# Performance work log

Measured on AMD Instinct MI355X. Metric: run time of the kernel, lower is better.

## Reference

```python
import jax, jax.numpy as jnp
import numpy as np

NUM_HEADS = 4
LN_EPS = 1e-5
L2_EPS = 1e-12


def setup_inputs() -> dict:
    key = jax.random.key(0)
    ks = jax.random.split(key, 10)
    B, L, D, Hd = 256, 197, 768, 512
    dh = Hd // NUM_HEADS  # 128
    NC = 1000
    sc = lambda k, shape, s: jax.random.normal(k, shape, jnp.float32) * s
    return {
        "cls_token": jax.random.normal(ks[0], (B, D), jnp.float32),
        "x": jax.random.normal(ks[1], (B, L, D), jnp.float32),
        "proj_w": sc(ks[2], (D, Hd), 0.02),
        "proj_b": jnp.zeros((Hd,), jnp.float32),
        "ln_g": jnp.ones((dh,), jnp.float32),
        "ln_b": jnp.zeros((dh,), jnp.float32),
        "conv1_w": sc(ks[3], (3, 3, 3, 3), 0.2),
        "conv2_w": sc(ks[4], (3, 3, 3, 3), 0.2),
        "cls1_w": sc(ks[5], (D, NC), 0.02),
        "cls1_b": jnp.zeros((NC,), jnp.float32),
        "cls2_w": sc(ks[6], (2883, NC), 0.02),
        "cls2_b": jnp.zeros((NC,), jnp.float32),
    }


def reference(cls_token, x, proj_w, proj_b, ln_g, ln_b, conv1_w, conv2_w,
              cls1_w, cls1_b, cls2_w, cls2_b):
    B, L, D = x.shape
    dh = ln_g.shape[0]
    # proj on patch tokens (drop cls at position 0)
    xp = x[:, 1:, :] @ proj_w + proj_b            # (B, 196, 512)
    Lp = xp.shape[1]
    H = xp.shape[2] // dh
    heads = xp.reshape(B, Lp, H, dh).transpose(2, 0, 1, 3)  # (H, B, Lp, dh)
    # LayerNorm over last dim (eps=1e-5, biased var, affine)
    mu = heads.mean(-1, keepdims=True)
    var = heads.var(-1, keepdims=True)
    hn = (heads - mu) * jax.lax.rsqrt(var + LN_EPS) * ln_g + ln_b
    # Covariance._remove_mean: adaptive_avg_pool2d on (B, dh, Lp) -> mean over BOTH dh and Lp per sample
    hn = hn - hn.mean(axis=(2, 3), keepdims=True)
    # 'near' cross-covariances between adjacent heads, all pairs batched
    x1, x2 = hn[:-1], hn[1:]                      # (H-1, B, Lp, dh)
    cov = jnp.einsum('pbnd,pbne->pbde', x1, x2) / Lp  # (H-1, B, dh, dh)
    # L2 normalize over dim=2 (row axis of each dh x dh map), F.normalize eps
    nrm = jnp.sqrt(jnp.sum(cov * cov, axis=2, keepdims=True))
    cov = cov / jnp.maximum(nrm, L2_EPS)
    cov = cov.transpose(1, 0, 2, 3)               # (B, 3, 128, 128)
    conv = lambda z, w: jax.lax.conv_general_dilated(
        z, w, (2, 2), 'VALID', dimension_numbers=('NCHW', 'OIHW', 'NCHW'))
    z = conv(cov, conv1_w)                        # (B, 3, 63, 63)
    z = jax.nn.gelu(z, approximate=False)
    z = conv(z, conv2_w)                          # (B, 3, 31, 31)
    flat = z.reshape(B, -1)                       # (B, 2883)
    out = ((cls_token @ cls1_w + cls1_b) + (flat @ cls2_w + cls2_b)) / 2
    return out
```

## Files before the change

kernel.cpp:

```cpp
#include <hip/hip_runtime.h>
#include <hip/hip_bf16.h>
#include <cstdint>

typedef __bf16 bf16_t;
typedef __bf16 bf16x4 __attribute__((ext_vector_type(4)));
typedef __bf16 bf16x8 __attribute__((ext_vector_type(8)));
typedef float floatx4 __attribute__((ext_vector_type(4)));

#define LNEPS 1e-5f

__device__ inline void async_copy16(const bf16_t* g, bf16_t* l) {
    __builtin_amdgcn_global_load_lds((const __attribute__((address_space(1))) void*)g,
                                     (__attribute__((address_space(3))) void*)l,
                                     16, 0, 0);
}

__global__ __launch_bounds__(256)
void k_cvt_x(const float* __restrict__ x, bf16_t* __restrict__ xbf) {
    const int vid = blockIdx.x * 256 + threadIdx.x;
    const int row = vid / 96;
    const int kv  = vid - row * 96;
    const int b = row / 196, l = row - (row / 196) * 196;
    const float* src = x + ((b * 197 + l + 1) * 96 + kv) * 8;
    const floatx4 f0 = *(const floatx4*)src;
    const floatx4 f1 = *(const floatx4*)(src + 4);
    bf16x8 o;
#pragma unroll
    for (int e = 0; e < 4; e++) { o[e] = (bf16_t)f0[e]; o[e+4] = (bf16_t)f1[e]; }
    *(bf16x8*)(xbf + vid * 8) = o;
}

__global__ __launch_bounds__(256)
void k_transpose_w(const float* __restrict__ w, bf16_t* __restrict__ wt) {
    __shared__ bf16_t tile[32][33];
    const int bx = blockIdx.x;
    const int by = blockIdx.y;
    const int tx = threadIdx.x & 31, ty = threadIdx.x >> 5;
    for (int i = ty; i < 32; i += 8)
        tile[i][tx] = (bf16_t)w[(by*32 + i)*512 + bx*32 + tx];
    __syncthreads();
    for (int i = ty; i < 32; i += 8)
        wt[(bx*32 + i)*768 + by*32 + tx] = tile[tx][i];
}

__global__ __launch_bounds__(256, 3)
void k_proj_ln(const bf16_t* __restrict__ xbf, const bf16_t* __restrict__ wt,
               const float* __restrict__ pb, const float* __restrict__ lng,
               const float* __restrict__ lnb, bf16_t* __restrict__ hn,
               float* __restrict__ csum)
{
    __shared__ bf16_t As[3][128*32];
    __shared__ bf16_t Bs[3][128*32];

    const int t = threadIdx.x;
    const int lane = t & 63;
    const int wv = t >> 6;
    const int q = lane >> 4;
    const int c = lane & 15;
    const int L = blockIdx.x;
    const int xcd = L & 7, slot = L >> 3;
    const int h = slot & 3;
    const int m0 = (xcd + 8 * (slot >> 2)) * 128;

    const int srow  = t >> 2;
    const int skoff = (t & 3) * 8;
    const bf16_t* ag = xbf + (m0 + srow) * 768 + skoff;
    const bf16_t* bg = wt + (h*128 + srow) * 768 + skoff;

#define STAGE(B, kk)                                                     \
    {                                                                    \
        const int kn_ = (kk) * 32;                                       \
        async_copy16(ag + kn_,          &As[B][t*8]);                    \
        async_copy16(ag + 64*768 + kn_, &As[B][2048 + t*8]);             \
        async_copy16(bg + kn_,          &Bs[B][t*8]);                    \
        async_copy16(bg + 64*768 + kn_, &Bs[B][2048 + t*8]);             \
    }

#define COMPUTE(B)                                                       \
    {                                                                    \
        bf16x8 af[2], bfr[8];                                            \
        _Pragma("unroll")                                                \
        for (int i = 0; i < 2; i++)                                      \
            af[i] = *(const bf16x8*)&As[B][(wv*32 + i*16 + c)*32 + q*8]; \
        _Pragma("unroll")                                                \
        for (int j = 0; j < 8; j++)                                      \
            bfr[j] = *(const bf16x8*)&Bs[B][(j*16 + c)*32 + q*8];        \
        _Pragma("unroll")                                                \
        for (int i = 0; i < 2; i++)                                      \
            _Pragma("unroll")                                            \
            for (int j = 0; j < 8; j++)                                  \
                acc[i][j] = __builtin_amdgcn_mfma_f32_16x16x32_bf16(af[i], bfr[j], acc[i][j], 0, 0, 0); \
    }

    floatx4 acc[2][8];
#pragma unroll
    for (int i = 0; i < 2; i++)
#pragma unroll
        for (int j = 0; j < 8; j++)
#pragma unroll
            for (int r = 0; r < 4; r++) acc[i][j][r] = 0.f;

    STAGE(0, 0);
    STAGE(1, 1);
    STAGE(2, 2);

    for (int ks = 0; ks < 22; ks++) {
        const int buf = ks % 3;
        asm volatile("s_waitcnt vmcnt(8)" ::: "memory");
        __builtin_amdgcn_s_barrier();
        COMPUTE(buf);
        __builtin_amdgcn_s_barrier();
        if (ks < 21) STAGE(buf, ks + 3);
    }
    asm volatile("s_waitcnt vmcnt(4)" ::: "memory");
    __builtin_amdgcn_s_barrier();
    COMPUTE(1);
    __builtin_amdgcn_s_barrier();
    asm volatile("s_waitcnt vmcnt(0)" ::: "memory");
    __builtin_amdgcn_s_barrier();
    COMPUTE(2);

#undef STAGE
#undef COMPUTE

    float bias[8], gg[8], bb[8];
#pragma unroll
    for (int j = 0; j < 8; j++) {
        const int d = j*16 + c;
        bias[j] = pb[h*128 + d];
        gg[j]   = lng[d];
        bb[j]   = lnb[d];
    }
    float cs0[8], cs1[8];
#pragma unroll
    for (int j = 0; j < 8; j++) { cs0[j] = 0.f; cs1[j] = 0.f; }
    const int b0 = m0 / 196;
    const int bL = (m0 + 127) / 196;
#pragma unroll
    for (int i = 0; i < 2; i++) {
#pragma unroll
        for (int r = 0; r < 4; r++) {
            float s = 0.f, s2 = 0.f;
#pragma unroll
            for (int j = 0; j < 8; j++) {
                const float v = acc[i][j][r] + bias[j];
                acc[i][j][r] = v;
                s += v; s2 += v*v;
            }
#pragma unroll
            for (int o = 1; o < 16; o <<= 1) { s += __shfl_xor(s, o); s2 += __shfl_xor(s2, o); }
            const float mu = s * (1.f/128.f);
            const float ms = s2 * (1.f/128.f);
            const float rstd = rsqrtf(ms - mu*mu + LNEPS);
            const int gm = m0 + wv*32 + i*16 + q*4 + r;
            const int bI = gm / 196, l = gm - bI*196;
            bf16_t* dst = hn + (((h*256 + bI)*196 + l) << 7);
            const bool first = (bI == b0);
#pragma unroll
            for (int j = 0; j < 8; j++) {
                const float v = (acc[i][j][r] - mu)*rstd*gg[j] + bb[j];
                dst[j*16 + c] = (bf16_t)v;
                cs0[j] += first ? v : 0.f;
                cs1[j] += first ? 0.f : v;
            }
        }
    }
    float* scr = (float*)As;
#pragma unroll
    for (int j = 0; j < 8; j++) {
        float s0 = cs0[j], s1 = cs1[j];
        s0 += __shfl_xor(s0, 16); s0 += __shfl_xor(s0, 32);
        s1 += __shfl_xor(s1, 16); s1 += __shfl_xor(s1, 32);
        if (q == 0) {
            scr[(wv*2 + 0)*128 + j*16 + c] = s0;
            scr[(wv*2 + 1)*128 + j*16 + c] = s1;
        }
    }
    __syncthreads();
    {
        const int bucket = t >> 7, d = t & 127;
        if (bucket == 0 || bL > b0) {
            const float s = scr[(0*2 + bucket)*128 + d] + scr[(1*2 + bucket)*128 + d]
                          + scr[(2*2 + bucket)*128 + d] + scr[(3*2 + bucket)*128 + d];
            atomicAdd(&csum[((h*256 + b0 + bucket) << 7) + d], s);
        }
    }
}

__global__ __launch_bounds__(256, 2)
void k_cov(const bf16_t* __restrict__ hn, const float* __restrict__ colsum,
           float* __restrict__ cov)
{
    __shared__ bf16_t x1s[128*40];
    __shared__ bf16_t x2s[128*40];
    __shared__ float rs1[128], rs2[128];
    __shared__ float colsq[2][128];
    __shared__ float nrm_inv[128];
    __shared__ float mu_s[2];

    const int t = threadIdx.x;
    const int lane = t & 63;
    const int wv = t >> 6;
    const int wr = wv >> 1, wc = wv & 1;
    const int q = lane >> 4;
    const int c = lane & 15;
    const int b = blockIdx.x;
    const int p = blockIdx.y;

    const bf16_t* X1 = hn + (((p*256 + b)*196) << 7);
    const bf16_t* X2 = hn + ((((p+1)*256 + b)*196) << 7);

    if (t < 128) rs1[t] = colsum[((p*256 + b) << 7) + t];
    else         rs2[t & 127] = colsum[(((p+1)*256 + b) << 7) + (t & 127)];
    __syncthreads();
    if (wv == 0) {
        float s = rs1[lane] + rs1[lane + 64];
#pragma unroll
        for (int o = 1; o < 64; o <<= 1) s += __shfl_xor(s, o);
        if (lane == 0) mu_s[0] = s * (1.f/(196.f*128.f));
    } else if (wv == 1) {
        float s = rs2[lane] + rs2[lane + 64];
#pragma unroll
        for (int o = 1; o < 64; o <<= 1) s += __shfl_xor(s, o);
        if (lane == 0) mu_s[1] = s * (1.f/(196.f*128.f));
    }

    floatx4 acc[4][4];
#pragma unroll
    for (int i = 0; i < 4; i++)
#pragma unroll
        for (int j = 0; j < 4; j++)
#pragma unroll
            for (int r = 0; r < 4; r++) acc[i][j][r] = 0.f;

    const int nl = t >> 3;
    const int d0 = (t & 7) * 16;

    for (int n0 = 0; n0 < 224; n0 += 32) {
        __syncthreads();
        const int n = n0 + nl;
        bf16x8 va, vb, wa, wb;
        if (n < 196) {
            const bf16_t* s1 = X1 + (n << 7) + d0;
            const bf16_t* s2 = X2 + (n << 7) + d0;
            va = *(const bf16x8*)s1;
            vb = *(const bf16x8*)(s1 + 8);
            wa = *(const bf16x8*)s2;
            wb = *(const bf16x8*)(s2 + 8);
        } else {
#pragma unroll
            for (int e = 0; e < 8; e++) {
                va[e] = (bf16_t)0.f; vb[e] = (bf16_t)0.f;
                wa[e] = (bf16_t)0.f; wb[e] = (bf16_t)0.f;
            }
        }
#pragma unroll
        for (int e = 0; e < 8; e++) {
            x1s[(d0 + e)*40 + nl]     = va[e];
            x1s[(d0 + 8 + e)*40 + nl] = vb[e];
            x2s[(d0 + e)*40 + nl]     = wa[e];
            x2s[(d0 + 8 + e)*40 + nl] = wb[e];
        }
        __syncthreads();
        bf16x8 af[4], bfr[4];
#pragma unroll
        for (int i = 0; i < 4; i++)
            af[i] = *(const bf16x8*)&x1s[(wr*64 + i*16 + c)*40 + q*8];
#pragma unroll
        for (int j = 0; j < 4; j++)
            bfr[j] = *(const bf16x8*)&x2s[(wc*64 + j*16 + c)*40 + q*8];
#pragma unroll
        for (int i = 0; i < 4; i++)
#pragma unroll
            for (int j = 0; j < 4; j++)
                acc[i][j] = __builtin_amdgcn_mfma_f32_16x16x32_bf16(af[i], bfr[j], acc[i][j], 0, 0, 0);
    }

    const float mu1 = mu_s[0], mu2 = mu_s[1];
    const float invL = 1.f/196.f;
    float csq[4] = {0.f, 0.f, 0.f, 0.f};
#pragma unroll
    for (int i = 0; i < 4; i++)
#pragma unroll
        for (int j = 0; j < 4; j++)
#pragma unroll
            for (int r = 0; r < 4; r++) {
                const int d = wr*64 + i*16 + q*4 + r;
                const int e = wc*64 + j*16 + c;
                const float v = acc[i][j][r]*invL - mu2*rs1[d]*invL - mu1*rs2[e]*invL + mu1*mu2;
                acc[i][j][r] = v;
                csq[j] += v*v;
            }
#pragma unroll
    for (int j = 0; j < 4; j++) {
        float s = csq[j];
        s += __shfl_xor(s, 16);
        s += __shfl_xor(s, 32);
        csq[j] = s;
    }
    if (q == 0) {
#pragma unroll
        for (int j = 0; j < 4; j++) colsq[wr][wc*64 + j*16 + c] = csq[j];
    }
    __syncthreads();
    if (t < 128) {
        const float nr = sqrtf(colsq[0][t] + colsq[1][t]);
        nrm_inv[t] = 1.f / fmaxf(nr, 1e-12f);
    }
    __syncthreads();
    float* dst = cov + ((long)b*3 + p)*16384;
#pragma unroll
    for (int i = 0; i < 4; i++)
#pragma unroll
        for (int j = 0; j < 4; j++) {
            const int e = wc*64 + j*16 + c;
            const float ni = nrm_inv[e];
#pragma unroll
            for (int r = 0; r < 4; r++) {
                const int d = wr*64 + i*16 + q*4 + r;
                dst[(d << 7) + e] = acc[i][j][r] * ni;
            }
        }
}

__global__ __launch_bounds__(256)
void k_convs(const float* __restrict__ cov, const float* __restrict__ w1,
             const float* __restrict__ w2, bf16_t* __restrict__ Xb)
{
    __shared__ float Z[3*33*63];
    __shared__ float W1s[81];
    __shared__ float W2s[81];
    const int t = threadIdx.x;
    const int b = blockIdx.x >> 1, half = blockIdx.x & 1;
    const int zy0 = half ? 32 : 0;
    const int nzy = half ? 31 : 33;
    const int y20 = half ? 16 : 0;
    const int ny2 = half ? 15 : 16;
    if (t < 81) { W1s[t] = w1[t]; W2s[t] = w2[t]; }
    __syncthreads();
    const float* C = cov + (long)b*3*16384;
    const int ztot = 3*nzy*63;
    for (int idx = t; idx < ztot; idx += 256) {
        const int o = idx / (nzy*63), rem = idx - o*(nzy*63);
        const int yl = rem / 63, xx = rem - yl*63;
        const int y = zy0 + yl;
        float a = 0.f;
#pragma unroll
        for (int i = 0; i < 3; i++) {
            const float* Ci = C + i*16384 + (2*y)*128 + 2*xx;
            const float* Wi = &W1s[o*27 + i*9];
            a += Ci[0]*Wi[0]   + Ci[1]*Wi[1]   + Ci[2]*Wi[2]
               + Ci[128]*Wi[3] + Ci[129]*Wi[4] + Ci[130]*Wi[5]
               + Ci[256]*Wi[6] + Ci[257]*Wi[7] + Ci[258]*Wi[8];
        }
        Z[o*2079 + yl*63 + xx] = 0.5f*a*(1.0f + erff(a*0.70710678118654752f));
    }
    __syncthreads();
    const int c2tot = 3*ny2*31;
    for (int idx = t; idx < c2tot; idx += 256) {
        const int o = idx / (ny2*31), rem = idx - o*(ny2*31);
        const int y2l = rem / 31, x2 = rem - y2l*31;
        float a = 0.f;
#pragma unroll
        for (int i = 0; i < 3; i++) {
            const float* Zi = Z + i*2079 + (2*y2l)*63 + 2*x2;
            const float* Wi = &W2s[(o*3+i)*9];
            a += Zi[0]*Wi[0]   + Zi[1]*Wi[1]   + Zi[2]*Wi[2]
               + Zi[63]*Wi[3]  + Zi[64]*Wi[4]  + Zi[65]*Wi[5]
               + Zi[126]*Wi[6] + Zi[127]*Wi[7] + Zi[128]*Wi[8];
        }
        const int oy2 = y20 + y2l;
        Xb[(long)b*3712 + 768 + o*961 + oy2*31 + x2] = (bf16_t)a;
    }
}

__global__ __launch_bounds__(256)
void k_cvt_cls(const float* __restrict__ cls, bf16_t* __restrict__ Xb,
               float* __restrict__ csum)
{
    const int t = threadIdx.x, b = blockIdx.x;
    for (int k = t; k < 768; k += 256)
        Xb[b*3712 + k] = (bf16_t)cls[b*768 + k];
    if (t < 61) Xb[b*3712 + 3651 + t] = (bf16_t)0.f;
    float* cz = csum + b*512;
    cz[t] = 0.f; cz[t + 256] = 0.f;
}

__global__ __launch_bounds__(256)
void k_cvt_w(const float* __restrict__ W1, const float* __restrict__ W2,
             bf16_t* __restrict__ Wb)
{
    __shared__ bf16_t tile[32][33];
    const int k0 = blockIdx.x * 32;
    const int n0 = blockIdx.y * 32;
    const int tx = threadIdx.x & 31, ty = threadIdx.x >> 5;
    for (int i = ty; i < 32; i += 8) {
        const int k = k0 + i, n = n0 + tx;
        float v = 0.f;
        if (n < 1000 && k < 3651)
            v = (k < 768) ? W1[k*1000 + n] : W2[(k-768)*1000 + n];
        tile[i][tx] = (bf16_t)v;
    }
    __syncthreads();
    for (int i = ty; i < 32; i += 8)
        Wb[(n0 + i)*3712 + k0 + tx] = tile[tx][i];
}

__global__ __launch_bounds__(256, 2)
void k_gemm_cls(const bf16_t* __restrict__ Xb, const bf16_t* __restrict__ Wb,
                float* __restrict__ partial)
{
    __shared__ bf16_t As[128*32];
    __shared__ bf16_t Bs[128*32];

    const int t = threadIdx.x;
    const int lane = t & 63;
    const int wv = t >> 6;
    const int wr = wv >> 1, wc = wv & 1;
    const int q = lane >> 4;
    const int c = lane & 15;
    const int nt = blockIdx.x;
    const int mt = blockIdx.y;
    const int sp = blockIdx.z;

    const int srow  = t >> 2;
    const int skoff = (t & 3) * 8;
    const int m0 = mt * 128, n0 = nt * 128;
    const int kbase = sp * 928;
    const bf16_t* ag0 = Xb + (m0 + srow) * 3712 + kbase + skoff;
    const bf16_t* ag1 = Xb + (m0 + srow + 64) * 3712 + kbase + skoff;
    const bf16_t* bg0 = Wb + (n0 + srow) * 3712 + kbase + skoff;
    const bf16_t* bg1 = Wb + (n0 + srow + 64) * 3712 + kbase + skoff;

    floatx4 acc[4][4];
#pragma unroll
    for (int i = 0; i < 4; i++)
#pragma unroll
        for (int j = 0; j < 4; j++)
#pragma unroll
            for (int r = 0; r < 4; r++) acc[i][j][r] = 0.f;

    for (int k0 = 0; k0 < 928; k0 += 32) {
        __syncthreads();
        async_copy16(ag0 + k0, &As[t*8]);
        async_copy16(ag1 + k0, &As[2048 + t*8]);
        async_copy16(bg0 + k0, &Bs[t*8]);
        async_copy16(bg1 + k0, &Bs[2048 + t*8]);
        __syncthreads();
        bf16x8 af[4], bfr[4];
#pragma unroll
        for (int i = 0; i < 4; i++)
            af[i] = *(const bf16x8*)&As[(wr*64 + i*16 + c)*32 + q*8];
#pragma unroll
        for (int j = 0; j < 4; j++)
            bfr[j] = *(const bf16x8*)&Bs[(wc*64 + j*16 + c)*32 + q*8];
#pragma unroll
        for (int i = 0; i < 4; i++)
#pragma unroll
            for (int j = 0; j < 4; j++)
                acc[i][j] = __builtin_amdgcn_mfma_f32_16x16x32_bf16(af[i], bfr[j], acc[i][j], 0, 0, 0);
    }

    float* base = partial + ((long)sp*256 + m0)*1024 + n0;
#pragma unroll
    for (int i = 0; i < 4; i++)
#pragma unroll
        for (int r = 0; r < 4; r++) {
            const int row = wr*64 + i*16 + q*4 + r;
#pragma unroll
            for (int j = 0; j < 4; j++)
                base[row*1024 + wc*64 + j*16 + c] = acc[i][j][r];
        }
}

__global__ __launch_bounds__(256)
void k_cls_fin(const float* __restrict__ partial, const float* __restrict__ b1,
               const float* __restrict__ b2, float* __restrict__ out)
{
    const int idx = blockIdx.x * 256 + threadIdx.x;
    const int m = idx / 1000, n = idx - m*1000;
    float s = partial[(m)*1024 + n] + partial[(256 + m)*1024 + n]
            + partial[(512 + m)*1024 + n] + partial[(768 + m)*1024 + n];
    out[idx] = 0.5f*(s + b1[n] + b2[n]);
}

extern "C" void kernel_launch(void* const* d_in, const int* in_sizes, int n_in,
                              void* d_out, int out_size, void* d_ws, size_t ws_size,
                              hipStream_t stream) {
    const float* cls = (const float*)d_in[0];
    const float* x   = (const float*)d_in[1];
    const float* pw  = (const float*)d_in[2];
    const float* pb  = (const float*)d_in[3];
    const float* lng = (const float*)d_in[4];
    const float* lnb = (const float*)d_in[5];
    const float* c1w = (const float*)d_in[6];
    const float* c2w = (const float*)d_in[7];
    const float* w1  = (const float*)d_in[8];
    const float* b1  = (const float*)d_in[9];
    const float* w2  = (const float*)d_in[10];
    const float* b2  = (const float*)d_in[11];

    char* ws = (char*)d_ws;
    bf16_t* hn    = (bf16_t*)(ws);
    bf16_t* xbf   = (bf16_t*)(ws + 51380224ull);
    float*  covb  = (float*) (ws + 51380224ull);
    bf16_t* wt    = (bf16_t*)(ws + 128450560ull);
    float*  csum  = (float*) (ws + 129236992ull);
    bf16_t* Xb    = (bf16_t*)(ws + 129761280ull);
    bf16_t* Wb    = (bf16_t*)(ws + 131661824ull);
    float*  part  = (float*) (ws + 139264000ull);
    float*  out   = (float*)d_out;

    k_transpose_w<<<dim3(16, 24), 256, 0, stream>>>(pw, wt);
    k_cvt_x<<<18816, 256, 0, stream>>>(x, xbf);
    k_cvt_cls<<<256, 256, 0, stream>>>(cls, Xb, csum);
    k_cvt_w<<<dim3(116, 32), 256, 0, stream>>>(w1, w2, Wb);
    k_proj_ln<<<1568, 256, 0, stream>>>(xbf, wt, pb, lng, lnb, hn, csum);
    k_cov<<<dim3(256, 3), 256, 0, stream>>>(hn, csum, covb);
    k_convs<<<512, 256, 0, stream>>>(covb, c1w, c2w, Xb);
    k_gemm_cls<<<dim3(8, 2, 4), 256, 0, stream>>>(Xb, Wb, part);
    k_cls_fin<<<1000, 256, 0, stream>>>(part, b1, b2, out);
}
```

Measured before the change: 422.4 us.

## Fuse fp32-to-bf16 conversion of x into projection GEMM A-tile loads

```diff
diff --git a/kernel.cpp b/kernel.cpp
--- a/kernel.cpp
+++ b/kernel.cpp
@@ -9,25 +9,10 @@
 
 #define LNEPS 1e-5f
 
-__device__ inline void async_copy16(const bf16_t* g, bf16_t* l) {
+__device__ inline void async_copy16(const void* g, void* l) {
     __builtin_amdgcn_global_load_lds((const __attribute__((address_space(1))) void*)g,
                                      (__attribute__((address_space(3))) void*)l,
                                      16, 0, 0);
-}
-
-__global__ __launch_bounds__(256)
-void k_cvt_x(const float* __restrict__ x, bf16_t* __restrict__ xbf) {
-    const int vid = blockIdx.x * 256 + threadIdx.x;
-    const int row = vid / 96;
-    const int kv  = vid - row * 96;
-    const int b = row / 196, l = row - (row / 196) * 196;
-    const float* src = x + ((b * 197 + l + 1) * 96 + kv) * 8;
-    const floatx4 f0 = *(const floatx4*)src;
-    const floatx4 f1 = *(const floatx4*)(src + 4);
-    bf16x8 o;
-#pragma unroll
-    for (int e = 0; e < 4; e++) { o[e] = (bf16_t)f0[e]; o[e+4] = (bf16_t)f1[e]; }
-    *(bf16x8*)(xbf + vid * 8) = o;
 }
 
 __global__ __launch_bounds__(256)
@@ -43,13 +28,13 @@
         wt[(bx*32 + i)*768 + by*32 + tx] = tile[tx][i];
 }
 
-__global__ __launch_bounds__(256, 3)
-void k_proj_ln(const bf16_t* __restrict__ xbf, const bf16_t* __restrict__ wt,
+__global__ __launch_bounds__(256, 2)
+void k_proj_ln(const float* __restrict__ x, const bf16_t* __restrict__ wt,
                const float* __restrict__ pb, const float* __restrict__ lng,
                const float* __restrict__ lnb, bf16_t* __restrict__ hn,
                float* __restrict__ csum)
 {
-    __shared__ bf16_t As[3][128*32];
+    __shared__ float  AsF[3][128*32];
     __shared__ bf16_t Bs[3][128*32];
 
     const int t = threadIdx.x;
@@ -62,34 +47,53 @@
     const int h = slot & 3;
     const int m0 = (xcd + 8 * (slot >> 2)) * 128;
 
-    const int srow  = t >> 2;
-    const int skoff = (t & 3) * 8;
-    const bf16_t* ag = xbf + (m0 + srow) * 768 + skoff;
-    const bf16_t* bg = wt + (h*128 + srow) * 768 + skoff;
+    const int arow_lo = (lane >> 3);
+    const int asrc_ch = (lane & 7) ^ (lane >> 3);
+    const float* agp[4];
+#pragma unroll
+    for (int n = 0; n < 4; n++) {
+        const int gm = m0 + wv*32 + n*8 + arow_lo;
+        const int ab = gm / 196, al = gm - ab*196;
+        agp[n] = x + (size_t)(ab*197 + al + 1) * 768 + asrc_ch * 4;
+    }
+    const int adst = wv*1024 + lane*4;
+
+    const bf16_t* bg = wt + (h*128 + (t >> 2)) * 768 + (t & 3) * 8;
+
+    const int o0 = (((2*q)     ^ (c & 7)) << 2);
+    const int o1 = (((2*q + 1) ^ (c & 7)) << 2);
 
 #define STAGE(B, kk)                                                     \
     {                                                                    \
-        const int kn_ = (kk) * 32;                                       \
-        async_copy16(ag + kn_,          &As[B][t*8]);                    \
-        async_copy16(ag + 64*768 + kn_, &As[B][2048 + t*8]);             \
-        async_copy16(bg + kn_,          &Bs[B][t*8]);                    \
-        async_copy16(bg + 64*768 + kn_, &Bs[B][2048 + t*8]);             \
+        _Pragma("unroll")                                                \
+        for (int n_ = 0; n_ < 4; n_++)                                   \
+            async_copy16(agp[n_] + (kk)*32, &AsF[B][adst + n_*256]);     \
+        async_copy16(bg + (kk)*32,          &Bs[B][t*8]);                \
+        async_copy16(bg + 64*768 + (kk)*32, &Bs[B][2048 + t*8]);         \
     }
 
 #define COMPUTE(B)                                                       \
     {                                                                    \
         bf16x8 af[2], bfr[8];                                            \
         _Pragma("unroll")                                                \
-        for (int i = 0; i < 2; i++)                                      \
-            af[i] = *(const bf16x8*)&As[B][(wv*32 + i*16 + c)*32 + q*8]; \
+        for (int i_ = 0; i_ < 2; i_++) {                                 \
+            const int ro_ = (wv*32 + i_*16 + c) * 32;                    \
+            const floatx4 fa_ = *(const floatx4*)&AsF[B][ro_ + o0];      \
+            const floatx4 fb_ = *(const floatx4*)&AsF[B][ro_ + o1];      \
+            _Pragma("unroll")                                            \
+            for (int e_ = 0; e_ < 4; e_++) {                             \
+                af[i_][e_]     = (bf16_t)fa_[e_];                        \
+                af[i_][4 + e_] = (bf16_t)fb_[e_];                        \
+            }                                                            \
+        }                                                                \
         _Pragma("unroll")                                                \
-        for (int j = 0; j < 8; j++)                                      \
-            bfr[j] = *(const bf16x8*)&Bs[B][(j*16 + c)*32 + q*8];        \
+        for (int j_ = 0; j_ < 8; j_++)                                   \
+            bfr[j_] = *(const bf16x8*)&Bs[B][(j_*16 + c)*32 + q*8];      \
         _Pragma("unroll")                                                \
-        for (int i = 0; i < 2; i++)                                      \
+        for (int i_ = 0; i_ < 2; i_++)                                   \
             _Pragma("unroll")                                            \
-            for (int j = 0; j < 8; j++)                                  \
-                acc[i][j] = __builtin_amdgcn_mfma_f32_16x16x32_bf16(af[i], bfr[j], acc[i][j], 0, 0, 0); \
+            for (int j_ = 0; j_ < 8; j_++)                               \
+                acc[i_][j_] = __builtin_amdgcn_mfma_f32_16x16x32_bf16(af[i_], bfr[j_], acc[i_][j_], 0, 0, 0); \
     }
 
     floatx4 acc[2][8];
@@ -106,13 +110,13 @@
 
     for (int ks = 0; ks < 22; ks++) {
         const int buf = ks % 3;
-        asm volatile("s_waitcnt vmcnt(8)" ::: "memory");
+        asm volatile("s_waitcnt vmcnt(12)" ::: "memory");
         __builtin_amdgcn_s_barrier();
         COMPUTE(buf);
         __builtin_amdgcn_s_barrier();
         if (ks < 21) STAGE(buf, ks + 3);
     }
-    asm volatile("s_waitcnt vmcnt(4)" ::: "memory");
+    asm volatile("s_waitcnt vmcnt(6)" ::: "memory");
     __builtin_amdgcn_s_barrier();
     COMPUTE(1);
     __builtin_amdgcn_s_barrier();
@@ -165,7 +169,7 @@
             }
         }
     }
-    float* scr = (float*)As;
+    float* scr = &AsF[0][0];
 #pragma unroll
     for (int j = 0; j < 8; j++) {
         float s0 = cs0[j], s1 = cs1[j];
@@ -502,7 +506,6 @@
 
     char* ws = (char*)d_ws;
     bf16_t* hn    = (bf16_t*)(ws);
-    bf16_t* xbf   = (bf16_t*)(ws + 51380224ull);
     float*  covb  = (float*) (ws + 51380224ull);
     bf16_t* wt    = (bf16_t*)(ws + 128450560ull);
     float*  csum  = (float*) (ws + 129236992ull);
@@ -512,10 +515,9 @@
     float*  out   = (float*)d_out;
 
     k_transpose_w<<<dim3(16, 24), 256, 0, stream>>>(pw, wt);
-    k_cvt_x<<<18816, 256, 0, stream>>>(x, xbf);
     k_cvt_cls<<<256, 256, 0, stream>>>(cls, Xb, csum);
     k_cvt_w<<<dim3(116, 32), 256, 0, stream>>>(w1, w2, Wb);
-    k_proj_ln<<<1568, 256, 0, stream>>>(xbf, wt, pb, lng, lnb, hn, csum);
+    k_proj_ln<<<1568, 256, 0, stream>>>(x, wt, pb, lng, lnb, hn, csum);
     k_cov<<<dim3(256, 3), 256, 0, stream>>>(hn, csum, covb);
     k_convs<<<512, 256, 0, stream>>>(covb, c1w, c2w, Xb);
     k_gemm_cls<<<dim3(8, 2, 4), 256, 0, stream>>>(Xb, Wb, part);
```

Result: slower. 436.0 us (+3.2%).
